# Optimization experiments

Hardware: AMD Instinct MI355X
Metric: run time of the kernel (lower is better)

## Reference

```python
import jax, jax.numpy as jnp
import numpy as np


def setup_inputs() -> dict:
    key = jax.random.key(0)
    k1, k2 = jax.random.split(key)
    B, P, N, M = 8, 32, 1024, 1024
    normalized_receptive_fields = jax.random.normal(k1, (B, P, N, 3), dtype=jnp.float32)
    reconstructed_points = jax.random.normal(k2, (B, P, M, 3), dtype=jnp.float32)
    return {
        "normalized_receptive_fields": normalized_receptive_fields,
        "reconstructed_points": reconstructed_points,
    }


def reference(normalized_receptive_fields, reconstructed_points):
    B, P, M, _ = reconstructed_points.shape
    N = normalized_receptive_fields.shape[2]
    # Faithful to torch: permute(0,1,3,2) then reshape(-1, M, 3).
    x = jnp.transpose(reconstructed_points, (0, 1, 3, 2)).reshape(-1, M, 3)  # (BP, M, 3)
    y = normalized_receptive_fields.reshape(-1, N, 3)                        # (BP, N, 3)
    xx = jnp.sum(x * x, axis=-1)                 # (BP, M)
    yy = jnp.sum(y * y, axis=-1)                 # (BP, N)
    xy = jnp.einsum('bmc,bnc->bmn', x, y)        # (BP, M, N)
    dist = xx[:, :, None] + yy[:, None, :] - 2.0 * xy  # (BP, M, N)
    min_x_to_y = jnp.min(dist, axis=2)           # (BP, M)
    min_y_to_x = jnp.min(dist, axis=1)           # (BP, N)
    return jnp.mean(min_x_to_y) + jnp.mean(min_y_to_x)
```

## Files before the change

kernel.cpp:

```cpp
#include <hip/hip_runtime.h>
#include <hip/hip_bf16.h>


#define MM 1024
#define NN 1024
#define THREADS 1024
#define NWAVES 16
#define ROWS_PER_WAVE 64
#define RB 4
#define CPL 16
#define FINF 3.4e38f

template <int CTRL>
__device__ __forceinline__ float dpp_ror_min(float v) {
    int vi = __float_as_int(v);
    int t  = __builtin_amdgcn_update_dpp(vi, vi, CTRL, 0xf, 0xf, true);
    return fminf(v, __int_as_float(t));
}

__device__ __forceinline__ float wave_min64(float v, int lane_xor32_addr) {
    v = dpp_ror_min<0x121>(v);
    v = dpp_ror_min<0x122>(v);
    v = dpp_ror_min<0x124>(v);
    v = dpp_ror_min<0x128>(v);
    int s = __builtin_amdgcn_ds_swizzle(__float_as_int(v), 0x401F);
    v = fminf(v, __int_as_float(s));
    int p = __builtin_amdgcn_ds_bpermute(lane_xor32_addr, __float_as_int(v));
    return fminf(v, __int_as_float(p));
}

__global__ __launch_bounds__(THREADS, 4)
void chamfer_kernel(const float* __restrict__ nrf,
                    const float* __restrict__ rp,
                    float* __restrict__ out,
                    float inv_bpm, float inv_bpn) {
    const int bp   = blockIdx.x;
    const int tid  = threadIdx.x;
    const int lane = tid & 63;
    const int wave = tid >> 6;
    const int xaddr32 = ((lane ^ 32) << 2);

    __shared__ float  rpS[MM * 3];
    __shared__ float4 xS[MM];
    __shared__ float4 yS[NN];
    __shared__ float  colminS[NWAVES][NN];
    __shared__ float  rowsumS[NWAVES];
    __shared__ float  csumS[NWAVES];

    const float* rpB = rp  + (size_t)bp * MM * 3;
    const float* yB  = nrf + (size_t)bp * NN * 3;

    for (int i = tid; i < MM * 3; i += THREADS) rpS[i] = rpB[i];
    {
        float a = yB[tid * 3 + 0];
        float b = yB[tid * 3 + 1];
        float c = yB[tid * 3 + 2];
        yS[tid] = make_float4(a, b, c, a * a + b * b + c * c);
    }
    __syncthreads();

    {
        const int k = 3 * tid;
        float a = rpS[((k + 0) & (MM - 1)) * 3 + ((k + 0) >> 10)];
        float b = rpS[((k + 1) & (MM - 1)) * 3 + ((k + 1) >> 10)];
        float c = rpS[((k + 2) & (MM - 1)) * 3 + ((k + 2) >> 10)];
        xS[tid] = make_float4(-2.0f * a, -2.0f * b, -2.0f * c,
                              a * a + b * b + c * c);
    }
    __syncthreads();

    float colmin[CPL];
    #pragma unroll
    for (int i = 0; i < CPL; ++i) colmin[i] = FINF;

    float rowsum = 0.0f;
    const int m0 = wave * ROWS_PER_WAVE;
    for (int r0 = 0; r0 < ROWS_PER_WAVE; r0 += RB) {
        float4 x[RB];
        #pragma unroll
        for (int j = 0; j < RB; ++j) x[j] = xS[m0 + r0 + j];

        float rmin[RB];
        #pragma unroll
        for (int j = 0; j < RB; ++j) rmin[j] = FINF;

        #pragma unroll
        for (int i = 0; i < CPL; ++i) {
            const float4 yv = yS[i * 64 + lane];
            float e[RB];
            #pragma unroll
            for (int j = 0; j < RB; ++j) {
                e[j] = __builtin_fmaf(x[j].x, yv.x,
                        __builtin_fmaf(x[j].y, yv.y,
                         __builtin_fmaf(x[j].z, yv.z, yv.w)));
                rmin[j] = fminf(rmin[j], e[j]);
            }
            float d01 = fminf(e[0] + x[0].w, e[1] + x[1].w);
            float d23 = fminf(e[2] + x[2].w, e[3] + x[3].w);
            colmin[i] = fminf(fminf(colmin[i], d01), d23);
        }

        #pragma unroll
        for (int j = 0; j < RB; ++j) rmin[j] = wave_min64(rmin[j], xaddr32);
        #pragma unroll
        for (int j = 0; j < RB; ++j) rowsum += x[j].w + rmin[j];
    }

    #pragma unroll
    for (int i = 0; i < CPL; ++i) colminS[wave][i * 64 + lane] = colmin[i];
    if (lane == 0) rowsumS[wave] = rowsum;
    __syncthreads();

    {
        const int n = tid;
        float cm = colminS[0][n];
        #pragma unroll
        for (int w = 1; w < NWAVES; ++w) cm = fminf(cm, colminS[w][n]);
        float csum = cm;
        #pragma unroll
        for (int off = 32; off > 0; off >>= 1)
            csum += __shfl_xor(csum, off, 64);
        if (lane == 0) csumS[wave] = csum;
    }
    __syncthreads();

    if (tid == 0) {
        float rs = 0.0f, cs = 0.0f;
        #pragma unroll
        for (int w = 0; w < NWAVES; ++w) { rs += rowsumS[w]; cs += csumS[w]; }
        atomicAdd(out, rs * inv_bpm + cs * inv_bpn);
    }
}

extern "C" void kernel_launch(void* const* d_in, const int* in_sizes, int n_in,
                              void* d_out, int out_size, void* d_ws, size_t ws_size,
                              hipStream_t stream) {
    const float* nrf = (const float*)d_in[0];
    const float* rp  = (const float*)d_in[1];
    float* out = (float*)d_out;

    const int BP = in_sizes[1] / (MM * 3);
    const float inv_bpm = 1.0f / (float)(BP * MM);
    const float inv_bpn = 1.0f / (float)(BP * NN);

    (void)hipMemsetAsync(out, 0, sizeof(float), stream);
    chamfer_kernel<<<BP, THREADS, 0, stream>>>(nrf, rp, out, inv_bpm, inv_bpn);
}
```

Before: 97.24 us.

## Compute pairwise distances with bf16x3-split MFMA matrix cores

Replaces the scalar FMA distance loop with 32x32x16 bf16 MFMA instructions. Each fp32 coordinate and squared norm is split into three bf16 terms so the products approximate fp32 accuracy, and the norms are folded into the K dimension. Row and column minima are then taken over the accumulator tiles. The block size also drops to 512 threads with a packed LDS layout. The aim is to move the dominant distance arithmetic onto matrix cores, at the cost of split/packing overhead, heavier register use and possible precision differences.

Measured after the change: 98.58 us. No clear change (+1.4%).

```diff
diff --git a/kernel.cpp b/kernel.cpp
--- a/kernel.cpp
+++ b/kernel.cpp
@@ -1,16 +1,48 @@
 #include <hip/hip_runtime.h>
-#include <hip/hip_bf16.h>
 
 
 #define MM 1024
 #define NN 1024
-#define THREADS 1024
-#define NWAVES 16
-#define ROWS_PER_WAVE 64
-#define RB 4
-#define CPL 16
+#define THREADS 512
+#define NWAVES 8
 #define FINF 3.4e38f
 
+typedef float f32x16 __attribute__((ext_vector_type(16)));
+typedef __bf16 bf16x8 __attribute__((ext_vector_type(8)));
+
+#define B_STRIDE 80
+#define A_STRIDE 64
+#define B_OFF 0
+#define A_OFF (NN * B_STRIDE)
+#define CW_OFF A_OFF
+#define RS_OFF (A_OFF + MM * A_STRIDE)
+#define RED_OFF (RS_OFF + 64)
+#define LDS_BYTES (RED_OFF + 64)
+
+__device__ __forceinline__ unsigned short bf16_rne(float v) {
+    unsigned u = __float_as_uint(v);
+    u = u + 0x7FFFu + ((u >> 16) & 1u);
+    return (unsigned short)(u >> 16);
+}
+__device__ __forceinline__ float bf16f(unsigned short h) {
+    return __uint_as_float(((unsigned)h) << 16);
+}
+struct S3 { unsigned short h0, h1, h2; };
+__device__ __forceinline__ S3 split3(float v) {
+    S3 o;
+    o.h0 = bf16_rne(v);
+    float r = v - bf16f(o.h0);
+    o.h1 = bf16_rne(r);
+    float r2 = r - bf16f(o.h1);
+    o.h2 = bf16_rne(r2);
+    return o;
+}
+__device__ __forceinline__ unsigned pk(unsigned short a, unsigned short b) {
+    return (unsigned)a | ((unsigned)b << 16);
+}
+__device__ __forceinline__ float min3f(float a, float b, float c) {
+    return fminf(fminf(a, b), c);
+}
 template <int CTRL>
 __device__ __forceinline__ float dpp_ror_min(float v) {
     int vi = __float_as_int(v);
@@ -18,116 +50,141 @@
     return fminf(v, __int_as_float(t));
 }
 
-__device__ __forceinline__ float wave_min64(float v, int lane_xor32_addr) {
-    v = dpp_ror_min<0x121>(v);
-    v = dpp_ror_min<0x122>(v);
-    v = dpp_ror_min<0x124>(v);
-    v = dpp_ror_min<0x128>(v);
-    int s = __builtin_amdgcn_ds_swizzle(__float_as_int(v), 0x401F);
-    v = fminf(v, __int_as_float(s));
-    int p = __builtin_amdgcn_ds_bpermute(lane_xor32_addr, __float_as_int(v));
-    return fminf(v, __int_as_float(p));
-}
-
-__global__ __launch_bounds__(THREADS, 4)
+__global__ __launch_bounds__(THREADS, 2)
 void chamfer_kernel(const float* __restrict__ nrf,
                     const float* __restrict__ rp,
                     float* __restrict__ out,
                     float inv_bpm, float inv_bpn) {
-    const int bp   = blockIdx.x;
-    const int tid  = threadIdx.x;
+    __shared__ __align__(16) unsigned char smem[LDS_BYTES];
+    unsigned char* Bb = smem + B_OFF;
+    unsigned short* As = (unsigned short*)(smem + A_OFF);
+    float* colW = (float*)(smem + CW_OFF);
+    float* rowsumS = (float*)(smem + RS_OFF);
+    float* redS = (float*)(smem + RED_OFF);
+
+    const int bp = blockIdx.x;
+    const int tid = threadIdx.x;
     const int lane = tid & 63;
     const int wave = tid >> 6;
-    const int xaddr32 = ((lane ^ 32) << 2);
-
-    __shared__ float  rpS[MM * 3];
-    __shared__ float4 xS[MM];
-    __shared__ float4 yS[NN];
-    __shared__ float  colminS[NWAVES][NN];
-    __shared__ float  rowsumS[NWAVES];
-    __shared__ float  csumS[NWAVES];
-
-    const float* rpB = rp  + (size_t)bp * MM * 3;
-    const float* yB  = nrf + (size_t)bp * NN * 3;
-
-    for (int i = tid; i < MM * 3; i += THREADS) rpS[i] = rpB[i];
-    {
-        float a = yB[tid * 3 + 0];
-        float b = yB[tid * 3 + 1];
-        float c = yB[tid * 3 + 2];
-        yS[tid] = make_float4(a, b, c, a * a + b * b + c * c);
-    }
-    __syncthreads();
-
-    {
-        const int k = 3 * tid;
-        float a = rpS[((k + 0) & (MM - 1)) * 3 + ((k + 0) >> 10)];
-        float b = rpS[((k + 1) & (MM - 1)) * 3 + ((k + 1) >> 10)];
-        float c = rpS[((k + 2) & (MM - 1)) * 3 + ((k + 2) >> 10)];
-        xS[tid] = make_float4(-2.0f * a, -2.0f * b, -2.0f * c,
-                              a * a + b * b + c * c);
-    }
-    __syncthreads();
-
-    float colmin[CPL];
-    #pragma unroll
-    for (int i = 0; i < CPL; ++i) colmin[i] = FINF;
+    const int l31 = lane & 31;
+    const int lh = lane >> 5;
+    const unsigned short ONE = 0x3F80;
+
+    const float* yB = nrf + (size_t)bp * NN * 3;
+    const float* xB = rp + (size_t)bp * MM * 3;
+
+    for (int c = tid; c < NN; c += THREADS) {
+        float y0 = yB[c * 3 + 0], y1 = yB[c * 3 + 1], y2 = yB[c * 3 + 2];
+        float yy = __builtin_fmaf(y0, y0, __builtin_fmaf(y1, y1, y2 * y2));
+        S3 b0 = split3(y0), b1 = split3(y1), b2 = split3(y2), q = split3(yy);
+        uint4* dst = (uint4*)(Bb + c * B_STRIDE);
+        dst[0] = make_uint4(pk(b0.h0, b0.h1), pk(b0.h0, b0.h1), pk(b0.h2, b0.h0), pk(b1.h0, b1.h1));
+        dst[1] = make_uint4(pk(b1.h0, b1.h1), pk(b1.h2, b1.h0), pk(b2.h0, b2.h1), pk(b2.h0, b2.h1));
+        dst[2] = make_uint4(pk(b2.h2, b2.h0), pk(ONE, ONE), pk(ONE, q.h0), pk(q.h1, q.h2));
+        dst[3] = make_uint4(pk(b0.h2, b0.h1), pk(b1.h2, b1.h1), pk(b2.h2, b2.h1), 0u);
+        dst[4] = make_uint4(0u, 0u, 0u, 0u);
+    }
+    for (int m = tid; m < MM; m += THREADS) {
+        int k = 3 * m;
+        float x0 = xB[((k    ) & (MM - 1)) * 3 + ((k    ) >> 10)];
+        float x1 = xB[((k + 1) & (MM - 1)) * 3 + ((k + 1) >> 10)];
+        float x2 = xB[((k + 2) & (MM - 1)) * 3 + ((k + 2) >> 10)];
+        float xx = __builtin_fmaf(x0, x0, __builtin_fmaf(x1, x1, x2 * x2));
+        S3 a0 = split3(-2.0f * x0), a1 = split3(-2.0f * x1), a2 = split3(-2.0f * x2);
+        S3 p = split3(xx);
+        uint4* dst = (uint4*)((unsigned char*)As + m * A_STRIDE);
+        dst[0] = make_uint4(pk(a0.h0, a0.h0), pk(a0.h1, a0.h1), pk(a0.h0, a0.h2), pk(a1.h0, a1.h0));
+        dst[1] = make_uint4(pk(a1.h1, a1.h1), pk(a1.h0, a1.h2), pk(a2.h0, a2.h0), pk(a2.h1, a2.h1));
+        dst[2] = make_uint4(pk(a2.h0, a2.h2), pk(p.h0, p.h1), pk(p.h2, ONE), pk(ONE, ONE));
+        dst[3] = make_uint4(pk(a0.h1, a0.h2), pk(a1.h1, a1.h2), pk(a2.h1, a2.h2), 0u);
+    }
+    __syncthreads();
+
+    const int m0 = wave * 128;
+    bf16x8 af[4][2];
+    #pragma unroll
+    for (int s = 0; s < 4; ++s) {
+        #pragma unroll
+        for (int h = 0; h < 2; ++h)
+            af[s][h] = *(const bf16x8*)(As + (m0 + s * 32 + l31) * 32 + h * 16 + lh * 8);
+    }
+    __syncthreads();
+
+    float rmin[4][16];
+    #pragma unroll
+    for (int s = 0; s < 4; ++s)
+        #pragma unroll
+        for (int j = 0; j < 16; ++j) rmin[s][j] = FINF;
+
+    f32x16 Z = {};
+    const unsigned char* bptr = Bb + l31 * B_STRIDE + lh * 16;
+    const int xaddr32 = (lane ^ 32) << 2;
+    float* colWrow = colW + wave * 1024;
+
+    bf16x8 bf0 = *(const bf16x8*)(bptr);
+    bf16x8 bf1 = *(const bf16x8*)(bptr + 32);
+    for (int t = 0; t < 32; ++t) {
+        const unsigned char* np = bptr + 32 * B_STRIDE;
+        bf16x8 nb0 = *(const bf16x8*)(np);
+        bf16x8 nb1 = *(const bf16x8*)(np + 32);
+
+        float cm = FINF;
+        #pragma unroll
+        for (int s = 0; s < 4; ++s) {
+            f32x16 acc = __builtin_amdgcn_mfma_f32_32x32x16_bf16(af[s][0], bf0, Z, 0, 0, 0);
+            acc = __builtin_amdgcn_mfma_f32_32x32x16_bf16(af[s][1], bf1, acc, 0, 0, 0);
+            #pragma unroll
+            for (int j = 0; j < 16; ++j) rmin[s][j] = fminf(rmin[s][j], acc[j]);
+            float u0 = min3f(acc[0], acc[1], acc[2]);
+            float u1 = min3f(acc[3], acc[4], acc[5]);
+            float u2 = min3f(acc[6], acc[7], acc[8]);
+            float u3 = min3f(acc[9], acc[10], acc[11]);
+            float u4 = min3f(acc[12], acc[13], acc[14]);
+            cm = fminf(cm, fminf(min3f(u0, u1, u2), min3f(u3, u4, acc[15])));
+        }
+        int pz = __builtin_amdgcn_ds_bpermute(xaddr32, __float_as_int(cm));
+        cm = fminf(cm, __int_as_float(pz));
+        if (lh == 0) colWrow[t * 32 + l31] = cm;
+
+        bf0 = nb0; bf1 = nb1; bptr = np;
+    }
 
     float rowsum = 0.0f;
-    const int m0 = wave * ROWS_PER_WAVE;
-    for (int r0 = 0; r0 < ROWS_PER_WAVE; r0 += RB) {
-        float4 x[RB];
-        #pragma unroll
-        for (int j = 0; j < RB; ++j) x[j] = xS[m0 + r0 + j];
-
-        float rmin[RB];
-        #pragma unroll
-        for (int j = 0; j < RB; ++j) rmin[j] = FINF;
-
-        #pragma unroll
-        for (int i = 0; i < CPL; ++i) {
-            const float4 yv = yS[i * 64 + lane];
-            float e[RB];
-            #pragma unroll
-            for (int j = 0; j < RB; ++j) {
-                e[j] = __builtin_fmaf(x[j].x, yv.x,
-                        __builtin_fmaf(x[j].y, yv.y,
-                         __builtin_fmaf(x[j].z, yv.z, yv.w)));
-                rmin[j] = fminf(rmin[j], e[j]);
-            }
-            float d01 = fminf(e[0] + x[0].w, e[1] + x[1].w);
-            float d23 = fminf(e[2] + x[2].w, e[3] + x[3].w);
-            colmin[i] = fminf(fminf(colmin[i], d01), d23);
+    #pragma unroll
+    for (int s = 0; s < 4; ++s) {
+        #pragma unroll
+        for (int j = 0; j < 16; ++j) {
+            float v = rmin[s][j];
+            v = dpp_ror_min<0x121>(v);
+            v = dpp_ror_min<0x122>(v);
+            v = dpp_ror_min<0x124>(v);
+            v = dpp_ror_min<0x128>(v);
+            int sw = __builtin_amdgcn_ds_swizzle(__float_as_int(v), 0x401F);
+            v = fminf(v, __int_as_float(sw));
+            rowsum += v;
         }
-
-        #pragma unroll
-        for (int j = 0; j < RB; ++j) rmin[j] = wave_min64(rmin[j], xaddr32);
-        #pragma unroll
-        for (int j = 0; j < RB; ++j) rowsum += x[j].w + rmin[j];
-    }
-
-    #pragma unroll
-    for (int i = 0; i < CPL; ++i) colminS[wave][i * 64 + lane] = colmin[i];
-    if (lane == 0) rowsumS[wave] = rowsum;
-    __syncthreads();
-
-    {
-        const int n = tid;
-        float cm = colminS[0][n];
-        #pragma unroll
-        for (int w = 1; w < NWAVES; ++w) cm = fminf(cm, colminS[w][n]);
-        float csum = cm;
-        #pragma unroll
-        for (int off = 32; off > 0; off >>= 1)
-            csum += __shfl_xor(csum, off, 64);
-        if (lane == 0) csumS[wave] = csum;
-    }
+    }
+    if (l31 == 0) rowsumS[wave * 2 + lh] = rowsum;
+    __syncthreads();
+
+    float csum = 0.0f;
+    for (int c = tid; c < NN; c += THREADS) {
+        float v = colW[c];
+        #pragma unroll
+        for (int w = 1; w < NWAVES; ++w) v = fminf(v, colW[w * 1024 + c]);
+        csum += v;
+    }
+    #pragma unroll
+    for (int off = 32; off > 0; off >>= 1) csum += __shfl_xor(csum, off, 64);
+    if (lane == 0) redS[wave] = csum;
     __syncthreads();
 
     if (tid == 0) {
         float rs = 0.0f, cs = 0.0f;
         #pragma unroll
-        for (int w = 0; w < NWAVES; ++w) { rs += rowsumS[w]; cs += csumS[w]; }
+        for (int w = 0; w < NWAVES; ++w) cs += redS[w];
+        #pragma unroll
+        for (int w = 0; w < 2 * NWAVES; ++w) rs += rowsumS[w];
         atomicAdd(out, rs * inv_bpm + cs * inv_bpn);
     }
 }
```
